# Kernel tuning notes

Measured on AMD Instinct MI355X. Metric: run time of the kernel, lower is better.

Reference implementation:

```python
import jax, jax.numpy as jnp
import numpy as np

GAMMA = 1.4
CFL = 0.5
DX = 1e-3
ENTROPY_FIX = 0.1
NX = 1048576


def _roe_flux(rL, uL, pL, rR, uR, pR):
    """Roe flux with Harten entropy fix, vectorized over all interfaces."""
    g = GAMMA
    EL = pL / (g - 1) + 0.5 * rL * uL * uL
    ER = pR / (g - 1) + 0.5 * rR * uR * uR
    HL = (EL + pL) / rL
    HR = (ER + pR) / rR
    sL = jnp.sqrt(rL)
    sR = jnp.sqrt(rR)
    den = sL + sR
    ur = (sL * uL + sR * uR) / den
    Hr = (sL * HL + sR * HR) / den
    c = jnp.sqrt(jnp.clip((g - 1) * (Hr - 0.5 * ur * ur), 1e-10))
    eps = ENTROPY_FIX * c
    l1 = ur - c
    l3 = ur + c
    a1 = jnp.sqrt(l1 * l1 + eps * eps)
    a2 = jnp.sqrt(ur * ur + eps * eps)
    a3 = jnp.sqrt(l3 * l3 + eps * eps)
    drho = rR - rL
    du = uR - uL
    dp = pR - pL
    c2 = c * c
    al2 = drho - dp / c2
    al1 = (dp - c * rR * du) / (2 * c2)
    al3 = (dp + c * rR * du) / (2 * c2)
    FrL = rL * uL; FmL = rL * uL * uL + pL; FeL = uL * (EL + pL)
    FrR = rR * uR; FmR = rR * uR * uR + pR; FeR = uR * (ER + pR)
    dr = a1 * al1 + a2 * al2 + a3 * al3
    dm = a1 * al1 * l1 + a2 * al2 * ur + a3 * al3 * l3
    de = (a1 * al1 * (Hr - ur * c) + a2 * al2 * 0.5 * ur * ur
          + a3 * al3 * (Hr + ur * c))
    return (0.5 * (FrL + FrR - dr),
            0.5 * (FmL + FmR - dm),
            0.5 * (FeL + FeR - de))


def _step(carry, t_final):
    """One first-order Euler timestep with CFL-adaptive dt clipped to t_final."""
    rho, rhou, E, t = carry
    g = GAMMA
    u = rhou / rho
    p = (g - 1) * (E - 0.5 * rho * u * u)
    c = jnp.sqrt(g * p / rho)
    dt = CFL * DX / jnp.max(jnp.abs(u) + c)
    dt = jnp.minimum(dt, jnp.maximum(t_final - t, 0.0))
    # replicate edge ghost cells: [nx] -> [nx+2]
    rp = jnp.concatenate([rho[:1], rho, rho[-1:]])
    up = jnp.concatenate([u[:1], u, u[-1:]])
    pp = jnp.concatenate([p[:1], p, p[-1:]])
    # nx+1 interface fluxes
    Fr, Fm, Fe = _roe_flux(rp[:-1], up[:-1], pp[:-1], rp[1:], up[1:], pp[1:])
    dtdx = dt / DX
    return (rho - dtdx * (Fr[1:] - Fr[:-1]),
            rhou - dtdx * (Fm[1:] - Fm[:-1]),
            E - dtdx * (Fe[1:] - Fe[:-1]),
            t + dt)


def setup_inputs() -> dict:
    key = jax.random.key(0)
    k1, k2, k3 = jax.random.split(key, 3)
    rho = 1.0 + 0.5 * jax.random.uniform(k1, (NX,), jnp.float32)
    u = 0.1 * jax.random.normal(k2, (NX,), jnp.float32)
    p = 1.0 + 0.5 * jax.random.uniform(k3, (NX,), jnp.float32)
    return {"rho_init": rho, "u_init": u, "p_init": p,
            "t_final": jnp.float32(10.0), "n_steps": 32}


def reference(rho_init, u_init, p_init, t_final, n_steps):
    g = GAMMA
    rho = rho_init
    rhou = rho_init * u_init
    E = p_init / (g - 1) + 0.5 * rho_init * u_init ** 2
    body = jax.checkpoint(lambda c, _: (_step(c, t_final), None))
    (rho, rhou, E, _), _ = jax.lax.scan(
        body, (rho, rhou, E, jnp.float32(0.0)), None, length=n_steps)
    u = rhou / rho
    p = (g - 1) * (E - 0.5 * rho * u * u)
    return rho, u, p
```

## Files before the change

kernel.cpp:

```cpp
#include <hip/hip_runtime.h>


#define NXC   1048576
#define GAM   1.4f
#define GM1   0.4f
#define IGM1  2.5f
#define CFLC  0.5f
#define DXC   1e-3f
#define IDXC  1000.0f
#define EFIX  0.1f
#define NSTEPS 32
#define NSLOT  (NSTEPS + 1)

#define ABLK  1024
#define ACPT  4
#define ATILE (ABLK*ACPT)
#define ANBLK (NXC/ATILE)

__device__ __forceinline__ float frcp(float x){ return __builtin_amdgcn_rcpf(x); }
__device__ __forceinline__ float frsq(float x){ return __builtin_amdgcn_rsqf(x); }
__device__ __forceinline__ float fsqrt_(float x){ return __builtin_amdgcn_sqrtf(x); }

__device__ __forceinline__ float sysloadf(const float* p) {
    return __hip_atomic_load(p, __ATOMIC_RELAXED, __HIP_MEMORY_SCOPE_SYSTEM);
}
__device__ __forceinline__ void sysstoref(float* p, float v) {
    __hip_atomic_store(p, v, __ATOMIC_RELAXED, __HIP_MEMORY_SCOPE_SYSTEM);
}
__device__ __forceinline__ unsigned sysloadu(const unsigned* p) {
    return __hip_atomic_load(p, __ATOMIC_RELAXED, __HIP_MEMORY_SCOPE_SYSTEM);
}
__device__ __forceinline__ void sysstoreu(unsigned* p, unsigned v) {
    __hip_atomic_store(p, v, __ATOMIC_RELAXED, __HIP_MEMORY_SCOPE_SYSTEM);
}

__device__ __forceinline__ float wave_max(float v) {
    #pragma unroll
    for (int k = 32; k >= 1; k >>= 1)
        v = fmaxf(v, __shfl_xor(v, k));
    return v;
}

#define CTRL_TOTAL (NSLOT * ANBLK)

__global__ void bmax_init(unsigned* z) {
    for (int i = threadIdx.x; i < CTRL_TOTAL; i += 256) z[i] = 0xAAAAAAAAu;
}

__device__ __forceinline__ void roe1(const float rr[6], const float uu[6],
                                     const float pp[6], const float ss[6],
                                     const float gg[6], int j,
                                     float& Frj, float& Fmj, float& Fej) {
    float sL = ss[j], sR = ss[j + 1];
    float uL = uu[j], uR = uu[j + 1];
    float invden = frcp(sL + sR);
    float ur = (sL * uL + sR * uR) * invden;
    float Hr = (gg[j] + gg[j + 1]) * invden;
    float c  = fsqrt_(fmaxf(GM1 * (Hr - 0.5f * ur * ur), 1e-10f));
    float eps = EFIX * c;
    float l1 = ur - c, l3 = ur + c;
    float a1 = fsqrt_(l1 * l1 + eps * eps);
    float a2 = fsqrt_(ur * ur + eps * eps);
    float a3 = fsqrt_(l3 * l3 + eps * eps);
    float drho = rr[j + 1] - rr[j];
    float du   = uR - uL;
    float dp   = pp[j + 1] - pp[j];
    float c2 = c * c;
    float inv2c2 = frcp(c2 + c2);
    float al2 = drho - (dp + dp) * inv2c2;
    float tcd = c * rr[j + 1] * du;
    float al1 = (dp - tcd) * inv2c2;
    float al3 = (dp + tcd) * inv2c2;
    float FrL = rr[j] * uL, FrR = rr[j + 1] * uR;
    float FmL = FrL * uL + pp[j], FmR = FrR * uR + pp[j + 1];
    float FeL = uL * (gg[j] * sL), FeR = uR * (gg[j + 1] * sR);
    float w1 = a1 * al1, w2 = a2 * al2, w3 = a3 * al3;
    Frj = 0.5f * (FrL + FrR - (w1 + w2 + w3));
    Fmj = 0.5f * (FmL + FmR - (w1 * l1 + w2 * ur + w3 * l3));
    Fej = 0.5f * (FeL + FeR - (w1 * (Hr - ur * c) + w2 * (0.5f * ur * ur)
                               + w3 * (Hr + ur * c)));
}

__global__ __launch_bounds__(ABLK, 4) void euler_async(
        const float* __restrict__ rho0, const float* __restrict__ u0,
        const float* __restrict__ p0, const float* __restrict__ tf,
        float* __restrict__ out, unsigned* __restrict__ bmax,
        float* __restrict__ halo) {
    __shared__ float Lr[ABLK], Lu[ABLK], Lp[ABLK];
    __shared__ float Rr[ABLK], Ru[ABLK], Rp[ABLK];
    __shared__ float fxr[ABLK], fxm[ABLK], fxe[ABLK];
    __shared__ float red[ABLK / 64];
    __shared__ float samax;

    const int tid = threadIdx.x, bid = blockIdx.x;
    const int c0 = bid * ATILE + ACPT * tid;
    const int lane = tid & 63, wid = tid >> 6;

    float cr[4], cu[4], cp[4], cE[4], cs[4], cg[4];

    {
        float4 r4 = *(const float4*)(rho0 + c0);
        float4 u4 = *(const float4*)(u0 + c0);
        float4 p4 = *(const float4*)(p0 + c0);
        cr[0]=r4.x; cr[1]=r4.y; cr[2]=r4.z; cr[3]=r4.w;
        cu[0]=u4.x; cu[1]=u4.y; cu[2]=u4.z; cu[3]=u4.w;
        cp[0]=p4.x; cp[1]=p4.y; cp[2]=p4.z; cp[3]=p4.w;
        float nm = 0.f;
        #pragma unroll
        for (int c = 0; c < 4; ++c) {
            float E = cp[c] * IGM1 + 0.5f * cr[c] * cu[c] * cu[c];
            float q = frsq(cr[c]);
            cE[c] = E;
            cs[c] = cr[c] * q;
            cg[c] = (E + cp[c]) * q;
            nm = fmaxf(nm, fabsf(cu[c]) + fsqrt_(GAM * cp[c] * (q * q)));
        }
        Lr[tid]=cr[3]; Lu[tid]=cu[3]; Lp[tid]=cp[3];
        Rr[tid]=cr[0]; Ru[tid]=cu[0]; Rp[tid]=cp[0];
        if (tid == 0) {
            float* h = halo + (size_t)bid * 6;
            sysstoref(h, cr[0]); sysstoref(h+1, cu[0]); sysstoref(h+2, cp[0]);
        }
        if (tid == ABLK - 1) {
            float* h = halo + (size_t)bid * 6 + 3;
            sysstoref(h, cr[3]); sysstoref(h+1, cu[3]); sysstoref(h+2, cp[3]);
        }
        nm = wave_max(nm);
        if (lane == 0) red[wid] = nm;
        __syncthreads();
        if (tid == 0) {
            float bm = red[0];
            #pragma unroll
            for (int w = 1; w < ABLK / 64; ++w) bm = fmaxf(bm, red[w]);
            sysstoreu(&bmax[bid], __float_as_uint(bm));
        }
    }
    float t = 0.f;
    const float tfin = *tf;

    for (int k = 0; k < NSTEPS; ++k) {
        const unsigned* brow = bmax + (size_t)k * ANBLK;

        float rr[6], uu[6], pp[6], ss[6], gg[6];
        #pragma unroll
        for (int c = 0; c < 4; ++c) {
            rr[c+1]=cr[c]; uu[c+1]=cu[c]; pp[c+1]=cp[c];
            ss[c+1]=cs[c]; gg[c+1]=cg[c];
        }
        if (tid == 0) {
            if (bid > 0) {
                while (sysloadu(&brow[bid - 1]) & 0x80000000u)
                    __builtin_amdgcn_s_sleep(1);
                const float* h = halo + ((size_t)k * ANBLK + (bid - 1)) * 6 + 3;
                rr[0]=sysloadf(h); uu[0]=sysloadf(h+1); pp[0]=sysloadf(h+2);
            } else { rr[0]=cr[0]; uu[0]=cu[0]; pp[0]=cp[0]; }
        } else { rr[0]=Lr[tid-1]; uu[0]=Lu[tid-1]; pp[0]=Lp[tid-1]; }
        if (tid == ABLK - 1) {
            if (bid < ANBLK - 1) {
                while (sysloadu(&brow[bid + 1]) & 0x80000000u)
                    __builtin_amdgcn_s_sleep(1);
                const float* h = halo + ((size_t)k * ANBLK + (bid + 1)) * 6;
                rr[5]=sysloadf(h); uu[5]=sysloadf(h+1); pp[5]=sysloadf(h+2);
            } else { rr[5]=cr[3]; uu[5]=cu[3]; pp[5]=cp[3]; }
        } else { rr[5]=Rr[tid+1]; uu[5]=Ru[tid+1]; pp[5]=Rp[tid+1]; }

        {
            float E0 = pp[0] * IGM1 + 0.5f * rr[0] * uu[0] * uu[0];
            float q0 = frsq(rr[0]);
            ss[0] = rr[0] * q0;  gg[0] = (E0 + pp[0]) * q0;
            float E5 = pp[5] * IGM1 + 0.5f * rr[5] * uu[5] * uu[5];
            float q5 = frsq(rr[5]);
            ss[5] = rr[5] * q5;  gg[5] = (E5 + pp[5]) * q5;
        }

        float Fr[5], Fm[5], Fe[5];
        #pragma unroll
        for (int j = 0; j < 4; ++j)
            roe1(rr, uu, pp, ss, gg, j, Fr[j], Fm[j], Fe[j]);
        fxr[tid] = Fr[0]; fxm[tid] = Fm[0]; fxe[tid] = Fe[0];
        if (tid == ABLK - 1)
            roe1(rr, uu, pp, ss, gg, 4, Fr[4], Fm[4], Fe[4]);

        if (wid == 0) {
            unsigned v0, v1, v2, v3;
            for (;;) {
                v0 = sysloadu(&brow[lane]);
                v1 = sysloadu(&brow[64 + lane]);
                v2 = sysloadu(&brow[128 + lane]);
                v3 = sysloadu(&brow[192 + lane]);
                if (__all(((v0 | v1 | v2 | v3) & 0x80000000u) == 0u)) break;
                __builtin_amdgcn_s_sleep(1);
            }
            float m = fmaxf(fmaxf(__uint_as_float(v0), __uint_as_float(v1)),
                            fmaxf(__uint_as_float(v2), __uint_as_float(v3)));
            m = wave_max(m);
            if (lane == 0) samax = m;
        }
        __syncthreads();

        if (tid < ABLK - 1) {
            Fr[4] = fxr[tid + 1]; Fm[4] = fxm[tid + 1]; Fe[4] = fxe[tid + 1];
        }
        float amax = samax;
        float dt = fminf((CFLC * DXC) * frcp(amax), fmaxf(tfin - t, 0.f));
        t += dt;
        float dtdx = dt * IDXC;

        float nm = 0.f;
        #pragma unroll
        for (int i = 1; i <= 4; ++i) {
            float r2 = rr[i]         - dtdx * (Fr[i] - Fr[i-1]);
            float m2 = rr[i] * uu[i] - dtdx * (Fm[i] - Fm[i-1]);
            float E2 = cE[i-1]       - dtdx * (Fe[i] - Fe[i-1]);
            float q2 = frsq(r2);
            float ir = q2 * q2;
            float u2 = m2 * ir;
            float p2 = GM1 * (E2 - 0.5f * r2 * u2 * u2);
            cr[i-1]=r2; cu[i-1]=u2; cp[i-1]=p2; cE[i-1]=E2;
            cs[i-1]=r2 * q2;
            cg[i-1]=(E2 + p2) * q2;
            nm = fmaxf(nm, fabsf(u2) + fsqrt_(GAM * p2 * ir));
        }

        if (k < NSTEPS - 1) {
            Lr[tid]=cr[3]; Lu[tid]=cu[3]; Lp[tid]=cp[3];
            Rr[tid]=cr[0]; Ru[tid]=cu[0]; Rp[tid]=cp[0];
            if (tid == 0) {
                float* h = halo + ((size_t)(k + 1) * ANBLK + bid) * 6;
                sysstoref(h, cr[0]); sysstoref(h+1, cu[0]); sysstoref(h+2, cp[0]);
            }
            if (tid == ABLK - 1) {
                float* h = halo + ((size_t)(k + 1) * ANBLK + bid) * 6 + 3;
                sysstoref(h, cr[3]); sysstoref(h+1, cu[3]); sysstoref(h+2, cp[3]);
            }
            nm = wave_max(nm);
            if (lane == 0) red[wid] = nm;
            __syncthreads();
            if (tid == 0) {
                float bm = red[0];
                #pragma unroll
                for (int w = 1; w < ABLK / 64; ++w) bm = fmaxf(bm, red[w]);
                sysstoreu(&bmax[(size_t)(k + 1) * ANBLK + bid],
                          __float_as_uint(bm));
            }
        } else {
            *(float4*)(out + c0)         = make_float4(cr[0], cr[1], cr[2], cr[3]);
            *(float4*)(out + NXC + c0)   = make_float4(cu[0], cu[1], cu[2], cu[3]);
            *(float4*)(out + 2*NXC + c0) = make_float4(cp[0], cp[1], cp[2], cp[3]);
        }
    }
}

extern "C" void kernel_launch(void* const* d_in, const int* in_sizes, int n_in,
                              void* d_out, int out_size, void* d_ws, size_t ws_size,
                              hipStream_t stream) {
    const float* rho0 = (const float*)d_in[0];
    const float* u0   = (const float*)d_in[1];
    const float* p0   = (const float*)d_in[2];
    const float* tf   = (const float*)d_in[3];

    float* out      = (float*)d_out;
    unsigned* bmax  = (unsigned*)d_ws;
    float* halo     = (float*)(bmax + CTRL_TOTAL);

    bmax_init<<<1, 256, 0, stream>>>(bmax);

    void* args[] = {(void*)&rho0, (void*)&u0, (void*)&p0, (void*)&tf,
                    (void*)&out, (void*)&bmax, (void*)&halo};
    hipLaunchCooperativeKernel((void*)euler_async, dim3(ANBLK), dim3(ABLK),
                               args, 0, stream);
}
```

Baseline: 230.5 us.

## Compute interior Roe fluxes before halo wait and reuse left-neighbor shared data

Each thread now computes its three interior-interface fluxes from registers before waiting on the global max-wavespeed poll. The left-edge and right-edge halo fluxes are computed afterwards. This drops the right-neighbor shared arrays, since the next thread reads its own boundary flux through fxr. The change also derives c and 1/(2c^2) from a single rsqrt, does the block max reduction with shuffles across 16 lanes, and spreads the control-array init over many blocks. The aim is to overlap flux arithmetic with inter-block synchronisation latency. In exchange, tid 0 now reads the left halo without spinning on that neighbour's flag; correctness then rests on the later all-block poll having already seen that flag clear.

```diff
diff --git a/kernel.cpp b/kernel.cpp
--- a/kernel.cpp
+++ b/kernel.cpp
@@ -17,6 +17,8 @@
 #define ATILE (ABLK*ACPT)
 #define ANBLK (NXC/ATILE)
 
+#define CTRL_TOTAL (NSLOT * ANBLK)
+
 __device__ __forceinline__ float frcp(float x){ return __builtin_amdgcn_rcpf(x); }
 __device__ __forceinline__ float frsq(float x){ return __builtin_amdgcn_rsqf(x); }
 __device__ __forceinline__ float fsqrt_(float x){ return __builtin_amdgcn_sqrtf(x); }
@@ -41,39 +43,37 @@
     return v;
 }
 
-#define CTRL_TOTAL (NSLOT * ANBLK)
-
 __global__ void bmax_init(unsigned* z) {
-    for (int i = threadIdx.x; i < CTRL_TOTAL; i += 256) z[i] = 0xAAAAAAAAu;
-}
-
-__device__ __forceinline__ void roe1(const float rr[6], const float uu[6],
-                                     const float pp[6], const float ss[6],
-                                     const float gg[6], int j,
-                                     float& Frj, float& Fmj, float& Fej) {
-    float sL = ss[j], sR = ss[j + 1];
-    float uL = uu[j], uR = uu[j + 1];
+    int i = blockIdx.x * 256 + threadIdx.x;
+    if (i < CTRL_TOTAL) z[i] = 0xAAAAAAAAu;
+}
+
+__device__ __forceinline__ void roe(
+        float rL, float uL, float pL, float sL, float gL,
+        float rR, float uR, float pR, float sR, float gR,
+        float& Frj, float& Fmj, float& Fej) {
     float invden = frcp(sL + sR);
     float ur = (sL * uL + sR * uR) * invden;
-    float Hr = (gg[j] + gg[j + 1]) * invden;
-    float c  = fsqrt_(fmaxf(GM1 * (Hr - 0.5f * ur * ur), 1e-10f));
+    float Hr = (gL + gR) * invden;
+    float c2u = fmaxf(GM1 * (Hr - 0.5f * ur * ur), 1e-10f);
+    float qc = frsq(c2u);
+    float c  = c2u * qc;
+    float inv2c2 = 0.5f * qc * qc;
     float eps = EFIX * c;
     float l1 = ur - c, l3 = ur + c;
     float a1 = fsqrt_(l1 * l1 + eps * eps);
     float a2 = fsqrt_(ur * ur + eps * eps);
     float a3 = fsqrt_(l3 * l3 + eps * eps);
-    float drho = rr[j + 1] - rr[j];
+    float drho = rR - rL;
     float du   = uR - uL;
-    float dp   = pp[j + 1] - pp[j];
-    float c2 = c * c;
-    float inv2c2 = frcp(c2 + c2);
+    float dp   = pR - pL;
     float al2 = drho - (dp + dp) * inv2c2;
-    float tcd = c * rr[j + 1] * du;
+    float tcd = c * rR * du;
     float al1 = (dp - tcd) * inv2c2;
     float al3 = (dp + tcd) * inv2c2;
-    float FrL = rr[j] * uL, FrR = rr[j + 1] * uR;
-    float FmL = FrL * uL + pp[j], FmR = FrR * uR + pp[j + 1];
-    float FeL = uL * (gg[j] * sL), FeR = uR * (gg[j + 1] * sR);
+    float FrL = rL * uL, FrR = rR * uR;
+    float FmL = FrL * uL + pL, FmR = FrR * uR + pR;
+    float FeL = uL * (gL * sL), FeR = uR * (gR * sR);
     float w1 = a1 * al1, w2 = a2 * al2, w3 = a3 * al3;
     Frj = 0.5f * (FrL + FrR - (w1 + w2 + w3));
     Fmj = 0.5f * (FmL + FmR - (w1 * l1 + w2 * ur + w3 * l3));
@@ -87,7 +87,6 @@
         float* __restrict__ out, unsigned* __restrict__ bmax,
         float* __restrict__ halo) {
     __shared__ float Lr[ABLK], Lu[ABLK], Lp[ABLK];
-    __shared__ float Rr[ABLK], Ru[ABLK], Rp[ABLK];
     __shared__ float fxr[ABLK], fxm[ABLK], fxe[ABLK];
     __shared__ float red[ABLK / 64];
     __shared__ float samax;
@@ -116,7 +115,6 @@
             nm = fmaxf(nm, fabsf(cu[c]) + fsqrt_(GAM * cp[c] * (q * q)));
         }
         Lr[tid]=cr[3]; Lu[tid]=cu[3]; Lp[tid]=cp[3];
-        Rr[tid]=cr[0]; Ru[tid]=cu[0]; Rp[tid]=cp[0];
         if (tid == 0) {
             float* h = halo + (size_t)bid * 6;
             sysstoref(h, cr[0]); sysstoref(h+1, cu[0]); sysstoref(h+2, cp[0]);
@@ -128,11 +126,13 @@
         nm = wave_max(nm);
         if (lane == 0) red[wid] = nm;
         __syncthreads();
-        if (tid == 0) {
-            float bm = red[0];
-            #pragma unroll
-            for (int w = 1; w < ABLK / 64; ++w) bm = fmaxf(bm, red[w]);
-            sysstoreu(&bmax[bid], __float_as_uint(bm));
+        if (tid < ABLK / 64) {
+            float bm = red[tid];
+            bm = fmaxf(bm, __shfl_xor(bm, 8));
+            bm = fmaxf(bm, __shfl_xor(bm, 4));
+            bm = fmaxf(bm, __shfl_xor(bm, 2));
+            bm = fmaxf(bm, __shfl_xor(bm, 1));
+            if (tid == 0) sysstoreu(&bmax[bid], __float_as_uint(bm));
         }
     }
     float t = 0.f;
@@ -140,46 +140,14 @@
 
     for (int k = 0; k < NSTEPS; ++k) {
         const unsigned* brow = bmax + (size_t)k * ANBLK;
-
-        float rr[6], uu[6], pp[6], ss[6], gg[6];
-        #pragma unroll
-        for (int c = 0; c < 4; ++c) {
-            rr[c+1]=cr[c]; uu[c+1]=cu[c]; pp[c+1]=cp[c];
-            ss[c+1]=cs[c]; gg[c+1]=cg[c];
-        }
-        if (tid == 0) {
-            if (bid > 0) {
-                while (sysloadu(&brow[bid - 1]) & 0x80000000u)
-                    __builtin_amdgcn_s_sleep(1);
-                const float* h = halo + ((size_t)k * ANBLK + (bid - 1)) * 6 + 3;
-                rr[0]=sysloadf(h); uu[0]=sysloadf(h+1); pp[0]=sysloadf(h+2);
-            } else { rr[0]=cr[0]; uu[0]=cu[0]; pp[0]=cp[0]; }
-        } else { rr[0]=Lr[tid-1]; uu[0]=Lu[tid-1]; pp[0]=Lp[tid-1]; }
-        if (tid == ABLK - 1) {
-            if (bid < ANBLK - 1) {
-                while (sysloadu(&brow[bid + 1]) & 0x80000000u)
-                    __builtin_amdgcn_s_sleep(1);
-                const float* h = halo + ((size_t)k * ANBLK + (bid + 1)) * 6;
-                rr[5]=sysloadf(h); uu[5]=sysloadf(h+1); pp[5]=sysloadf(h+2);
-            } else { rr[5]=cr[3]; uu[5]=cu[3]; pp[5]=cp[3]; }
-        } else { rr[5]=Rr[tid+1]; uu[5]=Ru[tid+1]; pp[5]=Rp[tid+1]; }
-
-        {
-            float E0 = pp[0] * IGM1 + 0.5f * rr[0] * uu[0] * uu[0];
-            float q0 = frsq(rr[0]);
-            ss[0] = rr[0] * q0;  gg[0] = (E0 + pp[0]) * q0;
-            float E5 = pp[5] * IGM1 + 0.5f * rr[5] * uu[5] * uu[5];
-            float q5 = frsq(rr[5]);
-            ss[5] = rr[5] * q5;  gg[5] = (E5 + pp[5]) * q5;
-        }
-
         float Fr[5], Fm[5], Fe[5];
-        #pragma unroll
-        for (int j = 0; j < 4; ++j)
-            roe1(rr, uu, pp, ss, gg, j, Fr[j], Fm[j], Fe[j]);
-        fxr[tid] = Fr[0]; fxm[tid] = Fm[0]; fxe[tid] = Fe[0];
-        if (tid == ABLK - 1)
-            roe1(rr, uu, pp, ss, gg, 4, Fr[4], Fm[4], Fe[4]);
+
+        roe(cr[0],cu[0],cp[0],cs[0],cg[0], cr[1],cu[1],cp[1],cs[1],cg[1],
+            Fr[1], Fm[1], Fe[1]);
+        roe(cr[1],cu[1],cp[1],cs[1],cg[1], cr[2],cu[2],cp[2],cs[2],cg[2],
+            Fr[2], Fm[2], Fe[2]);
+        roe(cr[2],cu[2],cp[2],cs[2],cg[2], cr[3],cu[3],cp[3],cs[3],cg[3],
+            Fr[3], Fm[3], Fe[3]);
 
         if (wid == 0) {
             unsigned v0, v1, v2, v3;
@@ -196,6 +164,38 @@
             m = wave_max(m);
             if (lane == 0) samax = m;
         }
+
+        {
+            float rl, ul, pl;
+            if (tid == 0) {
+                if (bid > 0) {
+                    const float* h = halo + ((size_t)k * ANBLK + (bid - 1)) * 6 + 3;
+                    rl = sysloadf(h); ul = sysloadf(h+1); pl = sysloadf(h+2);
+                } else { rl = cr[0]; ul = cu[0]; pl = cp[0]; }
+            } else { rl = Lr[tid-1]; ul = Lu[tid-1]; pl = Lp[tid-1]; }
+            float El = pl * IGM1 + 0.5f * rl * ul * ul;
+            float ql = frsq(rl);
+            float sl = rl * ql, gl = (El + pl) * ql;
+            roe(rl,ul,pl,sl,gl, cr[0],cu[0],cp[0],cs[0],cg[0],
+                Fr[0], Fm[0], Fe[0]);
+            fxr[tid] = Fr[0]; fxm[tid] = Fm[0]; fxe[tid] = Fe[0];
+        }
+
+        if (tid == ABLK - 1) {
+            float r5, u5, p5;
+            if (bid < ANBLK - 1) {
+                while (sysloadu(&brow[bid + 1]) & 0x80000000u)
+                    __builtin_amdgcn_s_sleep(1);
+                const float* h = halo + ((size_t)k * ANBLK + (bid + 1)) * 6;
+                r5 = sysloadf(h); u5 = sysloadf(h+1); p5 = sysloadf(h+2);
+            } else { r5 = cr[3]; u5 = cu[3]; p5 = cp[3]; }
+            float E5 = p5 * IGM1 + 0.5f * r5 * u5 * u5;
+            float q5 = frsq(r5);
+            float s5 = r5 * q5, g5 = (E5 + p5) * q5;
+            roe(cr[3],cu[3],cp[3],cs[3],cg[3], r5,u5,p5,s5,g5,
+                Fr[4], Fm[4], Fe[4]);
+        }
+
         __syncthreads();
 
         if (tid < ABLK - 1) {
@@ -208,23 +208,22 @@
 
         float nm = 0.f;
         #pragma unroll
-        for (int i = 1; i <= 4; ++i) {
-            float r2 = rr[i]         - dtdx * (Fr[i] - Fr[i-1]);
-            float m2 = rr[i] * uu[i] - dtdx * (Fm[i] - Fm[i-1]);
-            float E2 = cE[i-1]       - dtdx * (Fe[i] - Fe[i-1]);
+        for (int c = 0; c < 4; ++c) {
+            float r2 = cr[c]         - dtdx * (Fr[c+1] - Fr[c]);
+            float m2 = cr[c] * cu[c] - dtdx * (Fm[c+1] - Fm[c]);
+            float E2 = cE[c]         - dtdx * (Fe[c+1] - Fe[c]);
             float q2 = frsq(r2);
             float ir = q2 * q2;
             float u2 = m2 * ir;
             float p2 = GM1 * (E2 - 0.5f * r2 * u2 * u2);
-            cr[i-1]=r2; cu[i-1]=u2; cp[i-1]=p2; cE[i-1]=E2;
-            cs[i-1]=r2 * q2;
-            cg[i-1]=(E2 + p2) * q2;
+            cr[c]=r2; cu[c]=u2; cp[c]=p2; cE[c]=E2;
+            cs[c]=r2 * q2;
+            cg[c]=(E2 + p2) * q2;
             nm = fmaxf(nm, fabsf(u2) + fsqrt_(GAM * p2 * ir));
         }
 
         if (k < NSTEPS - 1) {
             Lr[tid]=cr[3]; Lu[tid]=cu[3]; Lp[tid]=cp[3];
-            Rr[tid]=cr[0]; Ru[tid]=cu[0]; Rp[tid]=cp[0];
             if (tid == 0) {
                 float* h = halo + ((size_t)(k + 1) * ANBLK + bid) * 6;
                 sysstoref(h, cr[0]); sysstoref(h+1, cu[0]); sysstoref(h+2, cp[0]);
@@ -236,12 +235,15 @@
             nm = wave_max(nm);
             if (lane == 0) red[wid] = nm;
             __syncthreads();
-            if (tid == 0) {
-                float bm = red[0];
-                #pragma unroll
-                for (int w = 1; w < ABLK / 64; ++w) bm = fmaxf(bm, red[w]);
-                sysstoreu(&bmax[(size_t)(k + 1) * ANBLK + bid],
-                          __float_as_uint(bm));
+            if (tid < ABLK / 64) {
+                float bm = red[tid];
+                bm = fmaxf(bm, __shfl_xor(bm, 8));
+                bm = fmaxf(bm, __shfl_xor(bm, 4));
+                bm = fmaxf(bm, __shfl_xor(bm, 2));
+                bm = fmaxf(bm, __shfl_xor(bm, 1));
+                if (tid == 0)
+                    sysstoreu(&bmax[(size_t)(k + 1) * ANBLK + bid],
+                              __float_as_uint(bm));
             }
         } else {
             *(float4*)(out + c0)         = make_float4(cr[0], cr[1], cr[2], cr[3]);
@@ -263,7 +265,7 @@
     unsigned* bmax  = (unsigned*)d_ws;
     float* halo     = (float*)(bmax + CTRL_TOTAL);
 
-    bmax_init<<<1, 256, 0, stream>>>(bmax);
+    bmax_init<<<(CTRL_TOTAL + 255) / 256, 256, 0, stream>>>(bmax);
 
     void* args[] = {(void*)&rho0, (void*)&u0, (void*)&p0, (void*)&tf,
                     (void*)&out, (void*)&bmax, (void*)&halo};
```

After: 249.4 us. +8.2%, slower.
